# Kernel tuning notes

Measured on AMD Instinct MI355X. Metric: run time of the kernel, lower is better.

Reference implementation:

```python
import jax, jax.numpy as jnp
import numpy as np

TEMPERATURE = 1.0
D_THRESH = 0.1
EPS = 1e-10
NORM_EPS = 1e-12  # F.normalize clamp


def _l2_normalize(x):
    n = jnp.sqrt(jnp.sum(x * x, axis=1, keepdims=True))
    return x / jnp.maximum(n, NORM_EPS)


def setup_inputs() -> dict:
    key = jax.random.key(0)
    k1, k2, k3 = jax.random.split(key, 3)
    N, D = 8192, 128
    f1 = jax.random.normal(k1, (N, D), dtype=jnp.float32)
    f2 = jax.random.normal(k2, (N, D), dtype=jnp.float32)
    # continuous targets in [-1, 1) so both the distance mask (|ti-tj|>0.1)
    # and the polarity mask (sign mismatch) are exercised
    targets = jax.random.uniform(k3, (N,), dtype=jnp.float32, minval=-1.0, maxval=1.0)
    return {"f1": f1, "f2": f2, "targets": targets}


def reference(f1, f2, targets):
    f1 = _l2_normalize(f1)
    f2 = _l2_normalize(f2)

    # self_mask: 1 where pair is a negative (far target or opposite polarity)
    dist_t = jnp.abs(targets[:, None] - targets[None, :])  # [N,N]
    mask_distance = dist_t > D_THRESH
    polarity = targets > 0
    mask_polarity = polarity[:, None] != polarity[None, :]
    self_mask = (mask_distance | mask_polarity).astype(f1.dtype)  # [N,N]

    # ||f1_i - f2_j||^2 via the cdist/matmul trick (avoids [N,N,D] tensor)
    sq1 = jnp.sum(f1 * f1, axis=1)  # [N]
    sq2 = jnp.sum(f2 * f2, axis=1)  # [N]
    dist = sq1[:, None] - 2.0 * (f1 @ f2.T) + sq2[None, :]  # [N,N]
    cos = 1.0 - 0.5 * dist

    p = jax.nn.softmax(cos / TEMPERATURE, axis=1)  # [N,N]
    pos_w = 1.0 - self_mask
    log_pos = -jnp.log(p + EPS) * pos_w
    log_neg = -jnp.log(1.0 - p + EPS) * self_mask
    per_row = (jnp.sum(log_pos, axis=1) / jnp.sum(pos_w, axis=1)
               + jnp.sum(log_neg, axis=1) / jnp.sum(self_mask, axis=1))
    return jnp.mean(per_row)
```

## Files before the change

kernel.cpp:

```cpp
#include <hip/hip_runtime.h>
#include <hip/hip_bf16.h>
#include <math.h>

#define NROWS 8192
#define DDIM  128
#define JCHUNKS 16
#define JPER  (NROWS / JCHUNKS)
#define STAGE_COLS 64
#define NSTAGES (JPER / STAGE_COLS)
#define ROWS_PER_BLOCK 128
#define GRIDX (NROWS / ROWS_PER_BLOCK)
#define NBUCK 1024

#define AS1 __attribute__((address_space(1)))
#define AS3 __attribute__((address_space(3)))

typedef __attribute__((ext_vector_type(8))) short bf16x8;
typedef __attribute__((ext_vector_type(4))) float f32x4;
typedef __attribute__((ext_vector_type(2))) float f32x2;

#define PB0 0.3678959f
#define PB1 0.3668905f
#define PB2 0.1836441f
#define PB3 0.0652423f
#define PB4 0.0161110f

__device__ inline f32x2 expcm1(f32x2 c) {
  f32x2 e = {PB4, PB4};
  e = e * c + (f32x2){PB3, PB3};
  e = e * c + (f32x2){PB2, PB2};
  e = e * c + (f32x2){PB1, PB1};
  e = e * c + (f32x2){PB0, PB0};
  return e;
}

__global__ __launch_bounds__(1024) void sort_kernel(
    const float* __restrict__ targets,
    int* __restrict__ pi, float* __restrict__ tps) {
  __shared__ int hist[NBUCK];
  __shared__ int scanb[NBUCK];
  __shared__ float tloc[NROWS];
  const int tid = threadIdx.x;
  hist[tid] = 0;
  __syncthreads();
  #pragma unroll
  for (int r = 0; r < NROWS / 1024; ++r) {
    float t = targets[r * 1024 + tid];
    int b = (int)((t + 1.0f) * (NBUCK / 2));
    b = min(max(b, 0), NBUCK - 1);
    atomicAdd(&hist[b], 1);
  }
  __syncthreads();
  int own = hist[tid];
  scanb[tid] = own;
  __syncthreads();
  for (int d = 1; d < NBUCK; d <<= 1) {
    int nv = scanb[tid];
    if (tid >= d) nv += scanb[tid - d];
    __syncthreads();
    scanb[tid] = nv;
    __syncthreads();
  }
  hist[tid] = scanb[tid] - own;
  __syncthreads();
  #pragma unroll
  for (int r = 0; r < NROWS / 1024; ++r) {
    int i = r * 1024 + tid;
    float t = targets[i];
    int b = (int)((t + 1.0f) * (NBUCK / 2));
    b = min(max(b, 0), NBUCK - 1);
    int pos = atomicAdd(&hist[b], 1);
    pi[pos] = i;
    tloc[pos] = t + (t > 0.0f ? 10.0f : -10.0f);
  }
  __syncthreads();
  #pragma unroll
  for (int r = 0; r < NROWS / 1024; ++r) {
    int i = r * 1024 + tid;
    tps[i] = tloc[i];
  }
}

__global__ __launch_bounds__(256) void norm_kernel(
    const float* __restrict__ f1, const float* __restrict__ f2,
    const int* __restrict__ pi,
    __hip_bfloat16* __restrict__ f1b, __hip_bfloat16* __restrict__ f2b,
    float* __restrict__ out) {
  if (blockIdx.x == 0 && threadIdx.x == 0) out[0] = 0.0f;
  int t = threadIdx.x;
  int rloc = t >> 5;
  int l = t & 31;
  int b = blockIdx.x;
  int half = (b >= NROWS / 8) ? 1 : 0;
  int row = (b - half * (NROWS / 8)) * 8 + rloc;
  int srow = pi[row];
  const float* src = half ? f2 : f1;
  __hip_bfloat16* dst = half ? f2b : f1b;

  float4 v = ((const float4*)src)[srow * (DDIM / 4) + l];
  float s = v.x * v.x + v.y * v.y + v.z * v.z + v.w * v.w;
  #pragma unroll
  for (int off = 1; off < 32; off <<= 1) s += __shfl_xor(s, off, 64);
  float inv = 1.0f / fmaxf(sqrtf(s), 1e-12f);
  __hip_bfloat16 hv[4];
  hv[0] = __float2bfloat16(v.x * inv);
  hv[1] = __float2bfloat16(v.y * inv);
  hv[2] = __float2bfloat16(v.z * inv);
  hv[3] = __float2bfloat16(v.w * inv);
  *(ushort4*)&dst[(size_t)row * DDIM + l * 4] = *(ushort4*)hv;
}

__global__ __launch_bounds__(256, 4) void stats_kernel(
    const __hip_bfloat16* __restrict__ f1b,
    const __hip_bfloat16* __restrict__ f2b,
    const float* __restrict__ tps,
    float* __restrict__ partials) {
  __shared__ __align__(16) char lds0[STAGE_COLS * 256];
  __shared__ __align__(16) char lds1[STAGE_COLS * 256];
  __shared__ __align__(16) float tsh[JPER];

  const int chunk = blockIdx.y;
  const int i0 = blockIdx.x * ROWS_PER_BLOCK;
  const int w    = threadIdx.x >> 6;
  const int lane = threadIdx.x & 63;
  const int p15  = lane & 15;
  const int rl4  = lane >> 4;
  const int rbase = i0 + w * 32;

  bf16x8 afrag[2][4];
  #pragma unroll
  for (int rs = 0; rs < 2; ++rs) {
    const __hip_bfloat16* arow =
        &f1b[(size_t)(rbase + rs * 16 + p15) * DDIM + rl4 * 8];
    #pragma unroll
    for (int ks = 0; ks < 4; ++ks)
      afrag[rs][ks] = *(const bf16x8*)(arow + ks * 32);
  }

  f32x2 tip2[4];
  #pragma unroll
  for (int rr = 0; rr < 4; ++rr) {
    tip2[rr][0] = tps[rbase + rl4 * 4 + rr];
    tip2[rr][1] = tps[rbase + 16 + rl4 * 4 + rr];
  }
  const float twmin = tps[rbase];
  const float twmax = tps[rbase + 31];

  f32x2 Z2[4]  = {{0,0},{0,0},{0,0},{0,0}};
  f32x2 Zp2[4] = {{0,0},{0,0},{0,0},{0,0}};
  f32x2 Cp2[4] = {{0,0},{0,0},{0,0},{0,0}};
  f32x2 Np2[4] = {{0,0},{0,0},{0,0},{0,0}};
  float posTiles = 0.0f;

  const int jb0 = chunk * JPER;

  int srcoff[4];
  #pragma unroll
  for (int q = 0; q < 4; ++q) {
    int rloc = w * 16 + q * 4 + rl4;
    int c    = p15 ^ (q * 4 + rl4);
    srcoff[q] = rloc * DDIM + c * 8;
  }

  #pragma unroll
  for (int rnd = 0; rnd < 2; ++rnd)
    __builtin_amdgcn_global_load_lds(
        (const AS1 void*)(tps + jb0 + rnd * 256 + w * 64 + lane),
        (AS3 void*)(&tsh[rnd * 256 + w * 64]), 4, 0, 0);
  {
    const __hip_bfloat16* gstage = f2b + (size_t)jb0 * DDIM;
    char* lbase = &lds0[w * 4096];
    #pragma unroll
    for (int q = 0; q < 4; ++q)
      __builtin_amdgcn_global_load_lds((const AS1 void*)(gstage + srcoff[q]),
                                       (AS3 void*)(lbase + q * 1024), 16, 0, 0);
  }

  for (int s = 0; s < NSTAGES; ++s) {
    __syncthreads();

    if (s + 1 < NSTAGES) {
      const __hip_bfloat16* gstage = f2b + (size_t)(jb0 + (s + 1) * STAGE_COLS) * DDIM;
      char* lbase = ((s + 1) & 1) ? &lds1[w * 4096] : &lds0[w * 4096];
      #pragma unroll
      for (int q = 0; q < 4; ++q)
        __builtin_amdgcn_global_load_lds((const AS1 void*)(gstage + srcoff[q]),
                                         (AS3 void*)(lbase + q * 1024), 16, 0, 0);
    }

    const char* lb = (s & 1) ? lds1 : lds0;
    #pragma unroll
    for (int ct = 0; ct < 4; ++ct) {
      const int rloc = ct * 16 + p15;
      bf16x8 bfrag[4];
      #pragma unroll
      for (int ks = 0; ks < 4; ++ks)
        bfrag[ks] = *(const bf16x8*)(lb + rloc * 256 + (((rl4 + ks * 4) ^ p15) << 4));

      f32x4 acc0 = {0.f, 0.f, 0.f, 0.f};
      f32x4 acc1 = {0.f, 0.f, 0.f, 0.f};
      #pragma unroll
      for (int ks = 0; ks < 4; ++ks) {
        acc0 = __builtin_amdgcn_mfma_f32_16x16x32_bf16(afrag[0][ks], bfrag[ks], acc0, 0, 0, 0);
        acc1 = __builtin_amdgcn_mfma_f32_16x16x32_bf16(afrag[1][ks], bfrag[ks], acc1, 0, 0, 0);
      }

      const int tb = s * STAGE_COLS + ct * 16;
      float jmn = tsh[tb], jmx = tsh[tb + 15];
      int uneg = __builtin_amdgcn_readfirstlane(
          ((jmn - twmax > 0.105f) || (twmin - jmx > 0.105f)) ? 1 : 0);
      int upos = __builtin_amdgcn_readfirstlane(
          ((twmax - jmn <= 0.095f) && (jmx - twmin <= 0.095f)) ? 1 : 0);

      if (uneg) {
        #pragma unroll
        for (int rr = 0; rr < 4; ++rr) {
          f32x2 c2 = {acc0[rr], acc1[rr]};
          Z2[rr] += expcm1(c2);
        }
      } else if (upos) {
        posTiles += 1.0f;
        #pragma unroll
        for (int rr = 0; rr < 4; ++rr) {
          f32x2 c2 = {acc0[rr], acc1[rr]};
          f32x2 e2 = expcm1(c2);
          Z2[rr]  += e2;
          Zp2[rr] += e2;
          Cp2[rr] += c2;
        }
      } else {
        float tj = tsh[tb + p15];
        f32x2 tj2 = {tj, tj};
        #pragma unroll
        for (int rr = 0; rr < 4; ++rr) {
          f32x2 c2 = {acc0[rr], acc1[rr]};
          f32x2 d2 = tip2[rr] - tj2;
          bool q0 = __builtin_fabsf(d2[0]) <= 0.1f;
          bool q1 = __builtin_fabsf(d2[1]) <= 0.1f;
          f32x2 m2 = {q0 ? 1.0f : 0.0f, q1 ? 1.0f : 0.0f};
          f32x2 e2 = expcm1(c2);
          Z2[rr]  += e2;
          Zp2[rr] += m2 * e2;
          Cp2[rr] += m2 * c2;
          Np2[rr] += m2;
        }
      }
    }
  }

  #pragma unroll
  for (int rr = 0; rr < 4; ++rr)
    Np2[rr] += (f32x2){posTiles, posTiles};

  #pragma unroll
  for (int rr = 0; rr < 4; ++rr) {
    for (int off = 1; off < 16; off <<= 1) {
      Z2[rr][0]  += __shfl_xor(Z2[rr][0],  off, 64);
      Z2[rr][1]  += __shfl_xor(Z2[rr][1],  off, 64);
      Zp2[rr][0] += __shfl_xor(Zp2[rr][0], off, 64);
      Zp2[rr][1] += __shfl_xor(Zp2[rr][1], off, 64);
      Cp2[rr][0] += __shfl_xor(Cp2[rr][0], off, 64);
      Cp2[rr][1] += __shfl_xor(Cp2[rr][1], off, 64);
      Np2[rr][0] += __shfl_xor(Np2[rr][0], off, 64);
      Np2[rr][1] += __shfl_xor(Np2[rr][1], off, 64);
    }
  }
  if (p15 == 0) {
    #pragma unroll
    for (int rs = 0; rs < 2; ++rs)
      #pragma unroll
      for (int rr = 0; rr < 4; ++rr) {
        size_t row = rbase + rs * 16 + rl4 * 4 + rr;
        f32x4 st = {Z2[rr][rs], Zp2[rr][rs], Cp2[rr][rs], Np2[rr][rs]};
        *(f32x4*)&partials[((size_t)row * JCHUNKS + chunk) * 4] = st;
      }
  }
}

__global__ void finalize_rows(const float* __restrict__ partials,
                              float* __restrict__ out) {
  int r = blockIdx.x * 256 + threadIdx.x;
  float Z = 0, Zp = 0, Cp = 0, Np = 0;
  for (int ch = 0; ch < JCHUNKS; ++ch) {
    float4 p = *(const float4*)&partials[((size_t)r * JCHUNKS + ch) * 4];
    Z += p.x; Zp += p.y; Cp += p.z; Np += p.w;
  }
  float Zn = Z - Zp;
  float nn = (float)NROWS - Np;
  float spos = (1.0f + logf(Z)) - Cp / Np;
  float sneg = Zn / Z - nn * 1e-10f;
  float per_row = spos + sneg / nn;

  float v = per_row;
  for (int off = 32; off; off >>= 1) v += __shfl_xor(v, off, 64);
  __shared__ float wsum[4];
  int lane = threadIdx.x & 63, wid = threadIdx.x >> 6;
  if (lane == 0) wsum[wid] = v;
  __syncthreads();
  if (threadIdx.x == 0)
    atomicAdd(out, (wsum[0] + wsum[1] + wsum[2] + wsum[3]) * (1.0f / (float)NROWS));
}

extern "C" void kernel_launch(void* const* d_in, const int* in_sizes, int n_in,
                              void* d_out, int out_size, void* d_ws, size_t ws_size,
                              hipStream_t stream) {
  const float* f1  = (const float*)d_in[0];
  const float* f2  = (const float*)d_in[1];
  const float* tgt = (const float*)d_in[2];
  float* out = (float*)d_out;

  char* ws = (char*)d_ws;
  __hip_bfloat16* f1b = (__hip_bfloat16*)ws;
  __hip_bfloat16* f2b = (__hip_bfloat16*)(ws + (size_t)NROWS * DDIM * 2);
  float* partials = (float*)(ws + (size_t)NROWS * DDIM * 4);
  int*   pi  = (int*)((char*)partials + (size_t)NROWS * JCHUNKS * 16);
  float* tps = (float*)((char*)pi + NROWS * 4);

  sort_kernel<<<1, 1024, 0, stream>>>(tgt, pi, tps);
  norm_kernel<<<2 * (NROWS / 8), 256, 0, stream>>>(f1, f2, pi, f1b, f2b, out);
  dim3 g2(GRIDX, JCHUNKS);
  stats_kernel<<<g2, 256, 0, stream>>>(f1b, f2b, tps, partials);
  finalize_rows<<<NROWS / 256, 256, 0, stream>>>(partials, out);
}
```

Baseline: 113.8 us.

## Widen stats tile to 64 rows per wave and split sort into histogram plus scatter

Each wave in the stats kernel now covers 64 rows (4 MFMA row tiles) instead of 32, so every B fragment read from LDS feeds four MFMAs and the f2 stream is loaded half as many times overall. The epilogue math is widened to 4-element vectors to match. This raises register use, and the occupancy hint drops from 4 to 2 blocks per CU, while the grid shrinks to 32x16 blocks. Separately, the single-block sort is split into a multi-block histogram kernel plus a scan/scatter kernel, with a memset for the global histogram. That adds launches but parallelises the histogram pass and drops the staging of sorted targets in LDS.

```diff
diff --git a/kernel.cpp b/kernel.cpp
--- a/kernel.cpp
+++ b/kernel.cpp
@@ -8,7 +8,7 @@
 #define JPER  (NROWS / JCHUNKS)
 #define STAGE_COLS 64
 #define NSTAGES (JPER / STAGE_COLS)
-#define ROWS_PER_BLOCK 128
+#define ROWS_PER_BLOCK 256
 #define GRIDX (NROWS / ROWS_PER_BLOCK)
 #define NBUCK 1024
 
@@ -17,7 +17,6 @@
 
 typedef __attribute__((ext_vector_type(8))) short bf16x8;
 typedef __attribute__((ext_vector_type(4))) float f32x4;
-typedef __attribute__((ext_vector_type(2))) float f32x2;
 
 #define PB0 0.3678959f
 #define PB1 0.3668905f
@@ -25,59 +24,58 @@
 #define PB3 0.0652423f
 #define PB4 0.0161110f
 
-__device__ inline f32x2 expcm1(f32x2 c) {
-  f32x2 e = {PB4, PB4};
-  e = e * c + (f32x2){PB3, PB3};
-  e = e * c + (f32x2){PB2, PB2};
-  e = e * c + (f32x2){PB1, PB1};
-  e = e * c + (f32x2){PB0, PB0};
+__device__ inline f32x4 expcm1_4(f32x4 c) {
+  f32x4 e = {PB4, PB4, PB4, PB4};
+  e = e * c + (f32x4){PB3, PB3, PB3, PB3};
+  e = e * c + (f32x4){PB2, PB2, PB2, PB2};
+  e = e * c + (f32x4){PB1, PB1, PB1, PB1};
+  e = e * c + (f32x4){PB0, PB0, PB0, PB0};
   return e;
 }
 
-__global__ __launch_bounds__(1024) void sort_kernel(
-    const float* __restrict__ targets,
+__device__ inline int bucket_of(float t) {
+  int b = (int)((t + 1.0f) * (NBUCK / 2));
+  return min(max(b, 0), NBUCK - 1);
+}
+
+__global__ __launch_bounds__(1024) void hist_kernel(
+    const float* __restrict__ targets, int* __restrict__ ghist) {
+  __shared__ int h[NBUCK];
+  const int tid = threadIdx.x;
+  h[tid] = 0;
+  __syncthreads();
+  float t = targets[blockIdx.x * 1024 + tid];
+  atomicAdd(&h[bucket_of(t)], 1);
+  __syncthreads();
+  int v = h[tid];
+  if (v) atomicAdd(&ghist[tid], v);
+}
+
+__global__ __launch_bounds__(1024) void scan_scatter_kernel(
+    const float* __restrict__ targets, const int* __restrict__ ghist,
     int* __restrict__ pi, float* __restrict__ tps) {
-  __shared__ int hist[NBUCK];
-  __shared__ int scanb[NBUCK];
-  __shared__ float tloc[NROWS];
+  __shared__ int sc[NBUCK];
+  __shared__ int cur[NBUCK];
   const int tid = threadIdx.x;
-  hist[tid] = 0;
-  __syncthreads();
-  #pragma unroll
-  for (int r = 0; r < NROWS / 1024; ++r) {
-    float t = targets[r * 1024 + tid];
-    int b = (int)((t + 1.0f) * (NBUCK / 2));
-    b = min(max(b, 0), NBUCK - 1);
-    atomicAdd(&hist[b], 1);
-  }
-  __syncthreads();
-  int own = hist[tid];
-  scanb[tid] = own;
+  int own = ghist[tid];
+  sc[tid] = own;
   __syncthreads();
   for (int d = 1; d < NBUCK; d <<= 1) {
-    int nv = scanb[tid];
-    if (tid >= d) nv += scanb[tid - d];
+    int v = sc[tid];
+    int add = (tid >= d) ? sc[tid - d] : 0;
     __syncthreads();
-    scanb[tid] = nv;
+    sc[tid] = v + add;
     __syncthreads();
   }
-  hist[tid] = scanb[tid] - own;
+  cur[tid] = sc[tid] - own;
   __syncthreads();
   #pragma unroll
   for (int r = 0; r < NROWS / 1024; ++r) {
     int i = r * 1024 + tid;
     float t = targets[i];
-    int b = (int)((t + 1.0f) * (NBUCK / 2));
-    b = min(max(b, 0), NBUCK - 1);
-    int pos = atomicAdd(&hist[b], 1);
+    int pos = atomicAdd(&cur[bucket_of(t)], 1);
     pi[pos] = i;
-    tloc[pos] = t + (t > 0.0f ? 10.0f : -10.0f);
-  }
-  __syncthreads();
-  #pragma unroll
-  for (int r = 0; r < NROWS / 1024; ++r) {
-    int i = r * 1024 + tid;
-    tps[i] = tloc[i];
+    tps[pos] = t + (t > 0.0f ? 10.0f : -10.0f);
   }
 }
 
@@ -110,7 +108,7 @@
   *(ushort4*)&dst[(size_t)row * DDIM + l * 4] = *(ushort4*)hv;
 }
 
-__global__ __launch_bounds__(256, 4) void stats_kernel(
+__global__ __launch_bounds__(256, 2) void stats_kernel(
     const __hip_bfloat16* __restrict__ f1b,
     const __hip_bfloat16* __restrict__ f2b,
     const float* __restrict__ tps,
@@ -125,11 +123,11 @@
   const int lane = threadIdx.x & 63;
   const int p15  = lane & 15;
   const int rl4  = lane >> 4;
-  const int rbase = i0 + w * 32;
-
-  bf16x8 afrag[2][4];
-  #pragma unroll
-  for (int rs = 0; rs < 2; ++rs) {
+  const int rbase = i0 + w * 64;
+
+  bf16x8 afrag[4][4];
+  #pragma unroll
+  for (int rs = 0; rs < 4; ++rs) {
     const __hip_bfloat16* arow =
         &f1b[(size_t)(rbase + rs * 16 + p15) * DDIM + rl4 * 8];
     #pragma unroll
@@ -137,19 +135,20 @@
       afrag[rs][ks] = *(const bf16x8*)(arow + ks * 32);
   }
 
-  f32x2 tip2[4];
-  #pragma unroll
-  for (int rr = 0; rr < 4; ++rr) {
-    tip2[rr][0] = tps[rbase + rl4 * 4 + rr];
-    tip2[rr][1] = tps[rbase + 16 + rl4 * 4 + rr];
-  }
+  f32x4 tip4[4];
+  #pragma unroll
+  for (int rr = 0; rr < 4; ++rr)
+    #pragma unroll
+    for (int rs = 0; rs < 4; ++rs)
+      tip4[rr][rs] = tps[rbase + rs * 16 + rl4 * 4 + rr];
+
   const float twmin = tps[rbase];
-  const float twmax = tps[rbase + 31];
-
-  f32x2 Z2[4]  = {{0,0},{0,0},{0,0},{0,0}};
-  f32x2 Zp2[4] = {{0,0},{0,0},{0,0},{0,0}};
-  f32x2 Cp2[4] = {{0,0},{0,0},{0,0},{0,0}};
-  f32x2 Np2[4] = {{0,0},{0,0},{0,0},{0,0}};
+  const float twmax = tps[rbase + 63];
+
+  f32x4 Z4[4]  = {};
+  f32x4 Zp4[4] = {};
+  f32x4 Cp4[4] = {};
+  f32x4 Np4[4] = {};
   float posTiles = 0.0f;
 
   const int jb0 = chunk * JPER;
@@ -197,13 +196,12 @@
       for (int ks = 0; ks < 4; ++ks)
         bfrag[ks] = *(const bf16x8*)(lb + rloc * 256 + (((rl4 + ks * 4) ^ p15) << 4));
 
-      f32x4 acc0 = {0.f, 0.f, 0.f, 0.f};
-      f32x4 acc1 = {0.f, 0.f, 0.f, 0.f};
-      #pragma unroll
-      for (int ks = 0; ks < 4; ++ks) {
-        acc0 = __builtin_amdgcn_mfma_f32_16x16x32_bf16(afrag[0][ks], bfrag[ks], acc0, 0, 0, 0);
-        acc1 = __builtin_amdgcn_mfma_f32_16x16x32_bf16(afrag[1][ks], bfrag[ks], acc1, 0, 0, 0);
-      }
+      f32x4 acc[4] = {};
+      #pragma unroll
+      for (int ks = 0; ks < 4; ++ks)
+        #pragma unroll
+        for (int rs = 0; rs < 4; ++rs)
+          acc[rs] = __builtin_amdgcn_mfma_f32_16x16x32_bf16(afrag[rs][ks], bfrag[ks], acc[rs], 0, 0, 0);
 
       const int tb = s * STAGE_COLS + ct * 16;
       float jmn = tsh[tb], jmx = tsh[tb + 15];
@@ -215,34 +213,33 @@
       if (uneg) {
         #pragma unroll
         for (int rr = 0; rr < 4; ++rr) {
-          f32x2 c2 = {acc0[rr], acc1[rr]};
-          Z2[rr] += expcm1(c2);
+          f32x4 c4 = {acc[0][rr], acc[1][rr], acc[2][rr], acc[3][rr]};
+          Z4[rr] += expcm1_4(c4);
         }
       } else if (upos) {
         posTiles += 1.0f;
         #pragma unroll
         for (int rr = 0; rr < 4; ++rr) {
-          f32x2 c2 = {acc0[rr], acc1[rr]};
-          f32x2 e2 = expcm1(c2);
-          Z2[rr]  += e2;
-          Zp2[rr] += e2;
-          Cp2[rr] += c2;
+          f32x4 c4 = {acc[0][rr], acc[1][rr], acc[2][rr], acc[3][rr]};
+          f32x4 e4 = expcm1_4(c4);
+          Z4[rr]  += e4;
+          Zp4[rr] += e4;
+          Cp4[rr] += c4;
         }
       } else {
         float tj = tsh[tb + p15];
-        f32x2 tj2 = {tj, tj};
         #pragma unroll
         for (int rr = 0; rr < 4; ++rr) {
-          f32x2 c2 = {acc0[rr], acc1[rr]};
-          f32x2 d2 = tip2[rr] - tj2;
-          bool q0 = __builtin_fabsf(d2[0]) <= 0.1f;
-          bool q1 = __builtin_fabsf(d2[1]) <= 0.1f;
-          f32x2 m2 = {q0 ? 1.0f : 0.0f, q1 ? 1.0f : 0.0f};
-          f32x2 e2 = expcm1(c2);
-          Z2[rr]  += e2;
-          Zp2[rr] += m2 * e2;
-          Cp2[rr] += m2 * c2;
-          Np2[rr] += m2;
+          f32x4 c4 = {acc[0][rr], acc[1][rr], acc[2][rr], acc[3][rr]};
+          f32x4 e4 = expcm1_4(c4);
+          f32x4 m4;
+          #pragma unroll
+          for (int rs = 0; rs < 4; ++rs)
+            m4[rs] = (__builtin_fabsf(tip4[rr][rs] - tj) <= 0.1f) ? 1.0f : 0.0f;
+          Z4[rr]  += e4;
+          Zp4[rr] += m4 * e4;
+          Cp4[rr] += m4 * c4;
+          Np4[rr] += m4;
         }
       }
     }
@@ -250,28 +247,27 @@
 
   #pragma unroll
   for (int rr = 0; rr < 4; ++rr)
-    Np2[rr] += (f32x2){posTiles, posTiles};
+    Np4[rr] += (f32x4){posTiles, posTiles, posTiles, posTiles};
 
   #pragma unroll
   for (int rr = 0; rr < 4; ++rr) {
     for (int off = 1; off < 16; off <<= 1) {
-      Z2[rr][0]  += __shfl_xor(Z2[rr][0],  off, 64);
-      Z2[rr][1]  += __shfl_xor(Z2[rr][1],  off, 64);
-      Zp2[rr][0] += __shfl_xor(Zp2[rr][0], off, 64);
-      Zp2[rr][1] += __shfl_xor(Zp2[rr][1], off, 64);
-      Cp2[rr][0] += __shfl_xor(Cp2[rr][0], off, 64);
-      Cp2[rr][1] += __shfl_xor(Cp2[rr][1], off, 64);
-      Np2[rr][0] += __shfl_xor(Np2[rr][0], off, 64);
-      Np2[rr][1] += __shfl_xor(Np2[rr][1], off, 64);
+      #pragma unroll
+      for (int rs = 0; rs < 4; ++rs) {
+        Z4[rr][rs]  += __shfl_xor(Z4[rr][rs],  off, 64);
+        Zp4[rr][rs] += __shfl_xor(Zp4[rr][rs], off, 64);
+        Cp4[rr][rs] += __shfl_xor(Cp4[rr][rs], off, 64);
+        Np4[rr][rs] += __shfl_xor(Np4[rr][rs], off, 64);
+      }
     }
   }
   if (p15 == 0) {
     #pragma unroll
-    for (int rs = 0; rs < 2; ++rs)
+    for (int rs = 0; rs < 4; ++rs)
       #pragma unroll
       for (int rr = 0; rr < 4; ++rr) {
         size_t row = rbase + rs * 16 + rl4 * 4 + rr;
-        f32x4 st = {Z2[rr][rs], Zp2[rr][rs], Cp2[rr][rs], Np2[rr][rs]};
+        f32x4 st = {Z4[rr][rs], Zp4[rr][rs], Cp4[rr][rs], Np4[rr][rs]};
         *(f32x4*)&partials[((size_t)row * JCHUNKS + chunk) * 4] = st;
       }
   }
@@ -313,10 +309,13 @@
   __hip_bfloat16* f1b = (__hip_bfloat16*)ws;
   __hip_bfloat16* f2b = (__hip_bfloat16*)(ws + (size_t)NROWS * DDIM * 2);
   float* partials = (float*)(ws + (size_t)NROWS * DDIM * 4);
-  int*   pi  = (int*)((char*)partials + (size_t)NROWS * JCHUNKS * 16);
-  float* tps = (float*)((char*)pi + NROWS * 4);
-
-  sort_kernel<<<1, 1024, 0, stream>>>(tgt, pi, tps);
+  int*   pi    = (int*)((char*)partials + (size_t)NROWS * JCHUNKS * 16);
+  float* tps   = (float*)((char*)pi + NROWS * 4);
+  int*   ghist = (int*)((char*)tps + NROWS * 4);
+
+  hipMemsetAsync(ghist, 0, NBUCK * sizeof(int), stream);
+  hist_kernel<<<NROWS / 1024, 1024, 0, stream>>>(tgt, ghist);
+  scan_scatter_kernel<<<1, 1024, 0, stream>>>(tgt, ghist, pi, tps);
   norm_kernel<<<2 * (NROWS / 8), 256, 0, stream>>>(f1, f2, pi, f1b, f2b, out);
   dim3 g2(GRIDX, JCHUNKS);
   stats_kernel<<<g2, 256, 0, stream>>>(f1b, f2b, tps, partials);
```

After: 240.5 us. +111.3%, slower.
